# Optimization experiments

Hardware: AMD Instinct MI355X
Metric: run time of the kernel (lower is better)

The kernel has to match this reference:

```python
import jax, jax.numpy as jnp
import numpy as np

N_NODES = 50000
D = 128
N_POS = 400000
N_NEG = 200000  # N_NODES * neg_k(4)
E = N_POS + N_NEG


def setup_inputs() -> dict:
    key = jax.random.key(0)
    k_x, k_w1, k_w2, k_p = jax.random.split(key, 4)
    x = jax.random.normal(k_x, (N_NODES, D), dtype=jnp.float32)
    # torch nn.Linear params: y = x @ W.T + b
    W1 = jax.random.normal(k_w1, (D, 2 * D), dtype=jnp.float32) * (1.0 / np.sqrt(2 * D))
    b1 = jnp.zeros((D,), dtype=jnp.float32)
    W2 = jax.random.normal(k_w2, (1, D), dtype=jnp.float32) * (1.0 / np.sqrt(D))
    b2 = jnp.zeros((1,), dtype=jnp.float32)
    pairs = jax.random.randint(k_p, (2, E), 0, N_NODES, dtype=jnp.int64)
    labels = jnp.concatenate([jnp.ones((N_POS,), jnp.float32), jnp.zeros((N_NEG,), jnp.float32)])
    return {"x": x, "W1": W1, "b1": b1, "W2": W2, "b2": b2, "labels": labels, "pairs": pairs}


def reference(x, W1, b1, W2, b2, labels, pairs):
    us, vs = pairs[0], pairs[1]
    # edge gather + concat: [E, 2D]
    feats = jnp.concatenate([x[us], x[vs]], axis=-1)
    h = jax.nn.relu(feats @ W1.T + b1)            # [E, D]
    z = (h @ W2.T + b2).ravel()                   # [E] logits
    # binary_cross_entropy_with_logits, mean reduction (numerically stable)
    loss = -jnp.mean(labels * jax.nn.log_sigmoid(z) + (1.0 - labels) * jax.nn.log_sigmoid(-z))
    return loss
```

## Files before the change

kernel.cpp:

```cpp
#include <hip/hip_runtime.h>
#include <hip/hip_fp16.h>

#define D 128
#define TWO_D 256

typedef _Float16 half2v __attribute__((ext_vector_type(2)));
typedef _Float16 half8v __attribute__((ext_vector_type(8)));
typedef float floatx4 __attribute__((ext_vector_type(4)));
typedef unsigned int uintx4 __attribute__((ext_vector_type(4)));

__device__ inline unsigned int pkrtz(float a, float b) {
    return __builtin_bit_cast(unsigned int, __builtin_amdgcn_cvt_pkrtz(a, b));
}

__global__ void build_wtf(const float* __restrict__ W1,
                          unsigned short* __restrict__ Wtf) {
    const int id = blockIdx.x * 256 + threadIdx.x;
    const int lane = id & 63, ks = (id >> 6) & 3, t = (id >> 8) & 3, w = id >> 10;
    const int quad = lane >> 4, l16 = lane & 15;
    const int o = w * 64 + t * 16 + l16;
    const float* wrow = (o < D) ? (W1 + (size_t)o * TWO_D)
                                : (W1 + (size_t)(o - D) * TWO_D + D);
    const float* wp = wrow + ks * 32 + quad * 8;
    floatx4 w0 = *(const floatx4*)wp;
    floatx4 w1v = *(const floatx4*)(wp + 4);
    uint4 pk;
    pk.x = pkrtz(w0[0], w0[1]);  pk.y = pkrtz(w0[2], w0[3]);
    pk.z = pkrtz(w1v[0], w1v[1]); pk.w = pkrtz(w1v[2], w1v[3]);
    *(uint4*)(Wtf + (size_t)id * 8) = pk;
}

__global__ __launch_bounds__(256) void gemm_nodes(
        const float* __restrict__ x, const unsigned short* __restrict__ Wtf,
        const float* __restrict__ b1,
        unsigned char* __restrict__ AB, float* __restrict__ out0, int nNodes) {
    const int tid  = threadIdx.x;
    const int wave = tid >> 6, lane = tid & 63;
    const int quad = lane >> 4, l16 = lane & 15;
    const int nb0  = blockIdx.x * 64;

    if (blockIdx.x == 0 && tid == 0) *out0 = 0.f;

    half8v Bf[4][4];
    float bias[4];
#pragma unroll
    for (int t = 0; t < 4; ++t) {
        const int o = wave * 64 + t * 16 + l16;
        bias[t] = (o < D) ? b1[o] : 0.f;
#pragma unroll
        for (int ks = 0; ks < 4; ++ks)
            Bf[t][ks] = *(const half8v*)(Wtf +
                ((size_t)(((wave * 4 + t) * 4 + ks) * 64) + lane) * 8);
    }

    __shared__ __align__(16) unsigned short xs[64][136];
    __shared__ __align__(16) float ct[2][16][260];

#pragma unroll
    for (int i = 0; i < 4; ++i) {
        const int c = tid + 256 * i;
        const int row = c >> 4, col8 = c & 15;
        const int node = nb0 + row;
        const int nc = node < nNodes ? node : nNodes - 1;
        const float* xp = x + (size_t)nc * D + col8 * 8;
        floatx4 v0 = *(const floatx4*)xp;
        floatx4 v1 = *(const floatx4*)(xp + 4);
        uint4 pk;
        pk.x = pkrtz(v0[0], v0[1]);  pk.y = pkrtz(v0[2], v0[3]);
        pk.z = pkrtz(v1[0], v1[1]);  pk.w = pkrtz(v1[2], v1[3]);
        *(uint4*)&xs[row][col8 * 8] = pk;
    }
    __syncthreads();

    const int srow = tid >> 4;
    const int sc8  = tid & 15;

    for (int sub = 0; sub < 4; ++sub) {
        half8v Af[4];
#pragma unroll
        for (int ks = 0; ks < 4; ++ks)
            Af[ks] = *(const half8v*)&xs[sub * 16 + l16][ks * 32 + quad * 8];

        floatx4 acc[4];
#pragma unroll
        for (int t = 0; t < 4; ++t) acc[t] = (floatx4){0.f, 0.f, 0.f, 0.f};
#pragma unroll
        for (int ks = 0; ks < 4; ++ks)
#pragma unroll
            for (int t = 0; t < 4; ++t)
                acc[t] = __builtin_amdgcn_mfma_f32_16x16x32_f16(Af[ks], Bf[t][ks], acc[t], 0, 0, 0);

        float (*cts)[260] = ct[sub & 1];
#pragma unroll
        for (int t = 0; t < 4; ++t) {
            const int o = wave * 64 + t * 16 + l16;
#pragma unroll
            for (int r = 0; r < 4; ++r)
                cts[quad * 4 + r][o] = acc[t][r] + bias[t];
        }
        __syncthreads();

        const int nrow = nb0 + sub * 16 + srow;
        if (nrow < nNodes) {
            floatx4 f0 = *(const floatx4*)&cts[srow][sc8 * 16];
            floatx4 f1 = *(const floatx4*)&cts[srow][sc8 * 16 + 4];
            floatx4 f2 = *(const floatx4*)&cts[srow][sc8 * 16 + 8];
            floatx4 f3 = *(const floatx4*)&cts[srow][sc8 * 16 + 12];
            uint4 o8;
            int d;
            d = __builtin_amdgcn_cvt_pk_fp8_f32(f0[0], f0[1], 0, false);
            d = __builtin_amdgcn_cvt_pk_fp8_f32(f0[2], f0[3], d, true);
            o8.x = (unsigned int)d;
            d = __builtin_amdgcn_cvt_pk_fp8_f32(f1[0], f1[1], 0, false);
            d = __builtin_amdgcn_cvt_pk_fp8_f32(f1[2], f1[3], d, true);
            o8.y = (unsigned int)d;
            d = __builtin_amdgcn_cvt_pk_fp8_f32(f2[0], f2[1], 0, false);
            d = __builtin_amdgcn_cvt_pk_fp8_f32(f2[2], f2[3], d, true);
            o8.z = (unsigned int)d;
            d = __builtin_amdgcn_cvt_pk_fp8_f32(f3[0], f3[1], 0, false);
            d = __builtin_amdgcn_cvt_pk_fp8_f32(f3[2], f3[3], d, true);
            o8.w = (unsigned int)d;
            *(uint4*)(AB + (size_t)nrow * TWO_D + sc8 * 16) = o8;
        }
    }
}

__device__ inline float dot4_fp8(unsigned int wa, unsigned int wb,
                                 unsigned int w2lo, unsigned int w2hi, float z) {
#if __has_builtin(__builtin_amdgcn_cvt_pk_f16_fp8)
    half2v a01 = __builtin_bit_cast(half2v, __builtin_amdgcn_cvt_pk_f16_fp8((short)(wa & 0xffffu)));
    half2v a23 = __builtin_bit_cast(half2v, __builtin_amdgcn_cvt_pk_f16_fp8((short)(wa >> 16)));
    half2v b01 = __builtin_bit_cast(half2v, __builtin_amdgcn_cvt_pk_f16_fp8((short)(wb & 0xffffu)));
    half2v b23 = __builtin_bit_cast(half2v, __builtin_amdgcn_cvt_pk_f16_fp8((short)(wb >> 16)));
    half2v zero = {(_Float16)0, (_Float16)0};
    half2v s01 = __builtin_elementwise_max(a01 + b01, zero);
    half2v s23 = __builtin_elementwise_max(a23 + b23, zero);
    z = __builtin_amdgcn_fdot2(s01, __builtin_bit_cast(half2v, w2lo), z, false);
    z = __builtin_amdgcn_fdot2(s23, __builtin_bit_cast(half2v, w2hi), z, false);
#else
    auto a01 = __builtin_amdgcn_cvt_pk_f32_fp8(wa, false);
    auto a23 = __builtin_amdgcn_cvt_pk_f32_fp8(wa, true);
    auto b01 = __builtin_amdgcn_cvt_pk_f32_fp8(wb, false);
    auto b23 = __builtin_amdgcn_cvt_pk_f32_fp8(wb, true);
    half2v wlo = __builtin_bit_cast(half2v, w2lo);
    half2v whi = __builtin_bit_cast(half2v, w2hi);
    float s0 = fmaxf(a01[0] + b01[0], 0.f), s1 = fmaxf(a01[1] + b01[1], 0.f);
    float s2 = fmaxf(a23[0] + b23[0], 0.f), s3 = fmaxf(a23[1] + b23[1], 0.f);
    z = fmaf(s0, (float)wlo[0], z); z = fmaf(s1, (float)wlo[1], z);
    z = fmaf(s2, (float)whi[0], z); z = fmaf(s3, (float)whi[1], z);
#endif
    return z;
}

__device__ inline float dot16(const uintx4 a4, const uintx4 b4,
                              const uintx4 w2a, const uintx4 w2b) {
    float z = 0.f;
    z = dot4_fp8(a4[0], b4[0], w2a[0], w2a[1], z);
    z = dot4_fp8(a4[1], b4[1], w2a[2], w2a[3], z);
    z = dot4_fp8(a4[2], b4[2], w2b[0], w2b[1], z);
    z = dot4_fp8(a4[3], b4[3], w2b[2], w2b[3], z);
    return z;
}

__device__ inline float red8(float z) {
    z += __shfl_xor(z, 4, 8);
    z += __shfl_xor(z, 2, 8);
    z += __shfl_xor(z, 1, 8);
    return z;
}

__device__ inline float bce(float z, float y) {
    const float t = __expf(-fabsf(z));
    return fmaxf(z, 0.f) - z * y + __logf(1.f + t);
}

__global__ __launch_bounds__(256) void edge_loss(
        const unsigned char* __restrict__ AB,
        const int* __restrict__ pairs,
        const float* __restrict__ labels,
        const float* __restrict__ W2,
        const float* __restrict__ b2,
        float* __restrict__ out, int E, float invE) {
    __shared__ unsigned int w2p[64];
    const int tid = threadIdx.x;
    if (tid < 64) {
        float2 w = *(const float2*)(W2 + tid * 2);
        half2v p = { (_Float16)w.x, (_Float16)w.y };
        w2p[tid] = __builtin_bit_cast(unsigned int, p);
    }
    __syncthreads();
    const int l8   = tid & 7;
    const uintx4 w2a = *(const uintx4*)&w2p[l8 * 8];
    const uintx4 w2b = *(const uintx4*)&w2p[l8 * 8 + 4];
    const float bb2 = b2[0];

    float acc = 0.f;
    const int group = (blockIdx.x * 256 + tid) >> 3;
    const int e0 = group * 8;
    if (e0 < E) {
        const int4 ua = *(const int4*)(pairs + e0);
        const int4 ub = *(const int4*)(pairs + e0 + 4);
        const int4 va = *(const int4*)(pairs + E + e0);
        const int4 vb = *(const int4*)(pairs + E + e0 + 4);
        const float lab = labels[e0 + l8];
        const int us[8] = {ua.x, ua.y, ua.z, ua.w, ub.x, ub.y, ub.z, ub.w};
        const int vs[8] = {va.x, va.y, va.z, va.w, vb.x, vb.y, vb.z, vb.w};

        unsigned int offA[8], offB[8];
#pragma unroll
        for (int k = 0; k < 8; ++k) {
            offA[k] = (unsigned int)us[k] * TWO_D + l8 * 16;
            offB[k] = (unsigned int)vs[k] * TWO_D + D + l8 * 16;
        }

        uintx4 A[8], B[8];
#pragma unroll
        for (int k = 0; k < 8; ++k) {
            asm volatile("global_load_dwordx4 %0, %1, %2"
                         : "=v"(A[k]) : "v"(offA[k]), "s"(AB) : "memory");
            asm volatile("global_load_dwordx4 %0, %1, %2"
                         : "=v"(B[k]) : "v"(offB[k]), "s"(AB) : "memory");
        }

        float z[8];
#define CONS2(k0, k1, cnt)                                                   \
        asm volatile("s_waitcnt vmcnt(" cnt ")" ::: "memory");               \
        __builtin_amdgcn_sched_barrier(0);                                   \
        z[k0] = red8(dot16(A[k0], B[k0], w2a, w2b));                         \
        z[k1] = red8(dot16(A[k1], B[k1], w2a, w2b));
        CONS2(0, 1, "12")
        CONS2(2, 3, "8")
        CONS2(4, 5, "4")
        CONS2(6, 7, "0")
#undef CONS2

        float zsel = z[0];
#pragma unroll
        for (int k = 1; k < 8; ++k)
            if (l8 == k) zsel = z[k];
        acc = bce(zsel + bb2, lab);
    }

#pragma unroll
    for (int m = 32; m >= 1; m >>= 1) acc += __shfl_xor(acc, m, 64);
    __shared__ float red[4];
    if ((tid & 63) == 0) red[tid >> 6] = acc;
    __syncthreads();
    if (tid == 0)
        atomicAdd(out, (red[0] + red[1] + red[2] + red[3]) * invE);
}

extern "C" void kernel_launch(void* const* d_in, const int* in_sizes, int n_in,
                              void* d_out, int out_size, void* d_ws, size_t ws_size,
                              hipStream_t stream) {
    const float* x      = (const float*)d_in[0];
    const float* W1     = (const float*)d_in[1];
    const float* b1     = (const float*)d_in[2];
    const float* W2     = (const float*)d_in[3];
    const float* b2     = (const float*)d_in[4];
    const float* labels = (const float*)d_in[5];
    const int*   pairs  = (const int*)d_in[6];

    const int nNodes = in_sizes[0] / D;
    const int E      = in_sizes[5];

    unsigned char*  AB  = (unsigned char*)d_ws;
    unsigned short* Wtf = (unsigned short*)((char*)d_ws + 13000704);

    build_wtf<<<16, 256, 0, stream>>>(W1, Wtf);
    gemm_nodes<<<(nNodes + 63) / 64, 256, 0, stream>>>(x, Wtf, b1, AB,
                                                        (float*)d_out, nNodes);
    const int nGroups = (E + 7) / 8;
    const int nBlocks = (nGroups + 31) / 32;
    edge_loss<<<nBlocks, 256, 0, stream>>>(AB, pairs, labels, W2, b2,
                                           (float*)d_out, E, 1.0f / (float)E);
}
```

Before: 125.1 us.

## Bucket edges by source-node bin so source features are staged in LDS

Result: slower. 170.7 us (+36.4%).

```diff
diff --git a/kernel.cpp b/kernel.cpp
--- a/kernel.cpp
+++ b/kernel.cpp
@@ -3,6 +3,14 @@
 
 #define D 128
 #define TWO_D 256
+#define BINW 128
+
+#define AB_OFF      0
+#define WTF_OFF     13000704
+#define HIST_OFF    13066240
+#define PSTART_OFF  13068288
+#define PCUR_OFF    13070336
+#define REC_OFF     13120512
 
 typedef _Float16 half2v __attribute__((ext_vector_type(2)));
 typedef _Float16 half8v __attribute__((ext_vector_type(8)));
@@ -14,8 +22,10 @@
 }
 
 __global__ void build_wtf(const float* __restrict__ W1,
-                          unsigned short* __restrict__ Wtf) {
+                          unsigned short* __restrict__ Wtf,
+                          int* __restrict__ hist, int nbins) {
     const int id = blockIdx.x * 256 + threadIdx.x;
+    if (id < nbins) hist[id] = 0;
     const int lane = id & 63, ks = (id >> 6) & 3, t = (id >> 8) & 3, w = id >> 10;
     const int quad = lane >> 4, l16 = lane & 15;
     const int o = w * 64 + t * 16 + l16;
@@ -124,6 +134,56 @@
         }
     }
 }
+
+
+__global__ __launch_bounds__(256) void hist_k(
+        const int* __restrict__ pairs, int* __restrict__ hist,
+        int E, int nbins) {
+    __shared__ int lh[512];
+    const int tid = threadIdx.x;
+    for (int i = tid; i < nbins; i += 256) lh[i] = 0;
+    __syncthreads();
+    const int stride = gridDim.x * 256;
+    for (int e = blockIdx.x * 256 + tid; e < E; e += stride)
+        atomicAdd(&lh[pairs[e] >> 7], 1);
+    __syncthreads();
+    for (int i = tid; i < nbins; i += 256)
+        if (lh[i]) atomicAdd(&hist[i], lh[i]);
+}
+
+__global__ __launch_bounds__(512) void scan_k(
+        const int* __restrict__ hist, int* __restrict__ pstart,
+        int* __restrict__ pcur, int nbins) {
+    __shared__ int sv[512];
+    const int t = threadIdx.x;
+    const int v = (t < nbins) ? ((hist[t] + 7) & ~7) : 0;
+    sv[t] = v;
+    for (int s = 1; s < 512; s <<= 1) {
+        __syncthreads();
+        const int a = (t >= s) ? sv[t - s] : 0;
+        __syncthreads();
+        sv[t] += a;
+    }
+    __syncthreads();
+    const int excl = sv[t] - v;
+    if (t < nbins) { pstart[t] = excl; pcur[t * 32] = excl; }
+}
+
+__global__ __launch_bounds__(256) void scatter_k(
+        const int* __restrict__ pairs, const float* __restrict__ labels,
+        int* __restrict__ pcur, unsigned int* __restrict__ rec,
+        int E) {
+    const int stride = gridDim.x * 256;
+    for (int e = blockIdx.x * 256 + threadIdx.x; e < E; e += stride) {
+        const int u = pairs[e];
+        const unsigned int v = (unsigned int)pairs[E + e];
+        const unsigned int lb = (labels[e] > 0.5f) ? 0x80000000u : 0u;
+        const int b = u >> 7;
+        const int slot = atomicAdd(&pcur[b * 32], 1);
+        rec[slot] = v | ((unsigned int)(u & 127) << 16) | lb;
+    }
+}
+
 
 __device__ inline float dot4_fp8(unsigned int wa, unsigned int wb,
                                  unsigned int w2lo, unsigned int w2hi, float z) {
@@ -176,69 +236,95 @@
 
 __global__ __launch_bounds__(256) void edge_loss(
         const unsigned char* __restrict__ AB,
-        const int* __restrict__ pairs,
-        const float* __restrict__ labels,
+        const unsigned int* __restrict__ rec,
+        const int* __restrict__ hist,
+        const int* __restrict__ pstart,
         const float* __restrict__ W2,
         const float* __restrict__ b2,
-        float* __restrict__ out, int E, float invE) {
+        float* __restrict__ out, int nNodes, float invE) {
+    const int tid = threadIdx.x;
+    const int b   = blockIdx.x >> 1;
+    const int h   = blockIdx.x & 1;
+
+    __shared__ __align__(16) unsigned char xs[BINW * 128];
     __shared__ unsigned int w2p[64];
-    const int tid = threadIdx.x;
+
     if (tid < 64) {
         float2 w = *(const float2*)(W2 + tid * 2);
         half2v p = { (_Float16)w.x, (_Float16)w.y };
         w2p[tid] = __builtin_bit_cast(unsigned int, p);
     }
-    __syncthreads();
-    const int l8   = tid & 7;
+    {
+        const int row = tid >> 1, half = tid & 1;
+        const size_t src = (size_t)(b * BINW + row) * TWO_D + half * 64;
+#pragma unroll
+        for (int j = 0; j < 4; ++j)
+            *(uint4*)&xs[tid * 64 + j * 16] =
+                *(const uint4*)(AB + src + j * 16);
+    }
+    __syncthreads();
+
+    const int l8 = tid & 7, tg = tid >> 3;
     const uintx4 w2a = *(const uintx4*)&w2p[l8 * 8];
     const uintx4 w2b = *(const uintx4*)&w2p[l8 * 8 + 4];
     const float bb2 = b2[0];
 
+    const int cnt = hist[b];
+    const int ps  = pstart[b];
+    const int ng  = (cnt + 7) >> 3;
+    const int nj  = (ng + 1 - h) >> 1;
+    const int nit = (nj + 31) >> 5;
+
     float acc = 0.f;
-    const int group = (blockIdx.x * 256 + tid) >> 3;
-    const int e0 = group * 8;
-    if (e0 < E) {
-        const int4 ua = *(const int4*)(pairs + e0);
-        const int4 ub = *(const int4*)(pairs + e0 + 4);
-        const int4 va = *(const int4*)(pairs + E + e0);
-        const int4 vb = *(const int4*)(pairs + E + e0 + 4);
-        const float lab = labels[e0 + l8];
-        const int us[8] = {ua.x, ua.y, ua.z, ua.w, ub.x, ub.y, ub.z, ub.w};
-        const int vs[8] = {va.x, va.y, va.z, va.w, vb.x, vb.y, vb.z, vb.w};
-
-        unsigned int offA[8], offB[8];
-#pragma unroll
-        for (int k = 0; k < 8; ++k) {
-            offA[k] = (unsigned int)us[k] * TWO_D + l8 * 16;
-            offB[k] = (unsigned int)vs[k] * TWO_D + D + l8 * 16;
-        }
-
-        uintx4 A[8], B[8];
-#pragma unroll
-        for (int k = 0; k < 8; ++k) {
-            asm volatile("global_load_dwordx4 %0, %1, %2"
-                         : "=v"(A[k]) : "v"(offA[k]), "s"(AB) : "memory");
+    for (int it = 0; it < nit; ++it) {
+        const int j  = it * 32 + tg;
+        const int jc = (j < nj) ? j : (nj - 1);
+        const int g  = 2 * jc + h;
+        const int slot0 = ps + g * 8;
+
+        const uint4 r0 = *(const uint4*)(rec + slot0);
+        const uint4 r1 = *(const uint4*)(rec + slot0 + 4);
+        const unsigned int rc[8] = {r0.x, r0.y, r0.z, r0.w,
+                                    r1.x, r1.y, r1.z, r1.w};
+
+        unsigned int offB[8];
+#pragma unroll
+        for (int k = 0; k < 8; ++k)
+            offB[k] = (rc[k] & 0xffffu) * TWO_D + D + l8 * 16;
+
+        uintx4 B[8];
+#pragma unroll
+        for (int k = 0; k < 8; ++k)
             asm volatile("global_load_dwordx4 %0, %1, %2"
                          : "=v"(B[k]) : "v"(offB[k]), "s"(AB) : "memory");
+
+        uintx4 A[8];
+#pragma unroll
+        for (int k = 0; k < 8; ++k) {
+            const int row = (rc[k] >> 16) & 127;
+            A[k] = *(const uintx4*)&xs[row * 128 + l8 * 16];
         }
 
         float z[8];
-#define CONS2(k0, k1, cnt)                                                   \
-        asm volatile("s_waitcnt vmcnt(" cnt ")" ::: "memory");               \
+#define CONS2(k0, k1, cnt_s)                                                 \
+        asm volatile("s_waitcnt vmcnt(" cnt_s ")" ::: "memory");             \
         __builtin_amdgcn_sched_barrier(0);                                   \
         z[k0] = red8(dot16(A[k0], B[k0], w2a, w2b));                         \
         z[k1] = red8(dot16(A[k1], B[k1], w2a, w2b));
-        CONS2(0, 1, "12")
-        CONS2(2, 3, "8")
-        CONS2(4, 5, "4")
+        CONS2(0, 1, "6")
+        CONS2(2, 3, "4")
+        CONS2(4, 5, "2")
         CONS2(6, 7, "0")
 #undef CONS2
 
         float zsel = z[0];
+        unsigned int rsel = rc[0];
 #pragma unroll
         for (int k = 1; k < 8; ++k)
-            if (l8 == k) zsel = z[k];
-        acc = bce(zsel + bb2, lab);
+            if (l8 == k) { zsel = z[k]; rsel = rc[k]; }
+        const float lab = (rsel & 0x80000000u) ? 1.f : 0.f;
+        const bool valid = (j < nj) && (g * 8 + l8 < cnt);
+        acc += valid ? bce(zsel + bb2, lab) : 0.f;
     }
 
 #pragma unroll
@@ -263,15 +349,23 @@
 
     const int nNodes = in_sizes[0] / D;
     const int E      = in_sizes[5];
-
-    unsigned char*  AB  = (unsigned char*)d_ws;
-    unsigned short* Wtf = (unsigned short*)((char*)d_ws + 13000704);
-
-    build_wtf<<<16, 256, 0, stream>>>(W1, Wtf);
+    const int nbins  = (nNodes + BINW - 1) / BINW;
+
+    char* ws = (char*)d_ws;
+    unsigned char*  AB     = (unsigned char*)(ws + AB_OFF);
+    unsigned short* Wtf    = (unsigned short*)(ws + WTF_OFF);
+    int*            hist   = (int*)(ws + HIST_OFF);
+    int*            pstart = (int*)(ws + PSTART_OFF);
+    int*            pcur   = (int*)(ws + PCUR_OFF);
+    unsigned int*   recp   = (unsigned int*)(ws + REC_OFF);
+
+    build_wtf<<<16, 256, 0, stream>>>(W1, Wtf, hist, nbins);
     gemm_nodes<<<(nNodes + 63) / 64, 256, 0, stream>>>(x, Wtf, b1, AB,
                                                         (float*)d_out, nNodes);
-    const int nGroups = (E + 7) / 8;
-    const int nBlocks = (nGroups + 31) / 32;
-    edge_loss<<<nBlocks, 256, 0, stream>>>(AB, pairs, labels, W2, b2,
-                                           (float*)d_out, E, 1.0f / (float)E);
-}
+    hist_k<<<256, 256, 0, stream>>>(pairs, hist, E, nbins);
+    scan_k<<<1, 512, 0, stream>>>(hist, pstart, pcur, nbins);
+    scatter_k<<<512, 256, 0, stream>>>(pairs, labels, pcur, recp, E);
+    edge_loss<<<nbins * 2, 256, 0, stream>>>(AB, recp, hist, pstart, W2, b2,
+                                             (float*)d_out, nNodes,
+                                             1.0f / (float)E);
+}
```

## Write fp8 node projections directly from MFMA registers with permuted column layout

Applied to the files above, without the earlier changes.

Result: no change. 126.3 us (+1.0%).

```diff
diff --git a/kernel.cpp b/kernel.cpp
--- a/kernel.cpp
+++ b/kernel.cpp
@@ -54,7 +54,6 @@
     }
 
     __shared__ __align__(16) unsigned short xs[64][136];
-    __shared__ __align__(16) float ct[2][16][260];
 
 #pragma unroll
     for (int i = 0; i < 4; ++i) {
@@ -72,9 +71,6 @@
     }
     __syncthreads();
 
-    const int srow = tid >> 4;
-    const int sc8  = tid & 15;
-
     for (int sub = 0; sub < 4; ++sub) {
         half8v Af[4];
 #pragma unroll
@@ -90,37 +86,18 @@
             for (int t = 0; t < 4; ++t)
                 acc[t] = __builtin_amdgcn_mfma_f32_16x16x32_f16(Af[ks], Bf[t][ks], acc[t], 0, 0, 0);
 
-        float (*cts)[260] = ct[sub & 1];
-#pragma unroll
-        for (int t = 0; t < 4; ++t) {
-            const int o = wave * 64 + t * 16 + l16;
-#pragma unroll
-            for (int r = 0; r < 4; ++r)
-                cts[quad * 4 + r][o] = acc[t][r] + bias[t];
-        }
-        __syncthreads();
-
-        const int nrow = nb0 + sub * 16 + srow;
-        if (nrow < nNodes) {
-            floatx4 f0 = *(const floatx4*)&cts[srow][sc8 * 16];
-            floatx4 f1 = *(const floatx4*)&cts[srow][sc8 * 16 + 4];
-            floatx4 f2 = *(const floatx4*)&cts[srow][sc8 * 16 + 8];
-            floatx4 f3 = *(const floatx4*)&cts[srow][sc8 * 16 + 12];
-            uint4 o8;
-            int d;
-            d = __builtin_amdgcn_cvt_pk_fp8_f32(f0[0], f0[1], 0, false);
-            d = __builtin_amdgcn_cvt_pk_fp8_f32(f0[2], f0[3], d, true);
-            o8.x = (unsigned int)d;
-            d = __builtin_amdgcn_cvt_pk_fp8_f32(f1[0], f1[1], 0, false);
-            d = __builtin_amdgcn_cvt_pk_fp8_f32(f1[2], f1[3], d, true);
-            o8.y = (unsigned int)d;
-            d = __builtin_amdgcn_cvt_pk_fp8_f32(f2[0], f2[1], 0, false);
-            d = __builtin_amdgcn_cvt_pk_fp8_f32(f2[2], f2[3], d, true);
-            o8.z = (unsigned int)d;
-            d = __builtin_amdgcn_cvt_pk_fp8_f32(f3[0], f3[1], 0, false);
-            d = __builtin_amdgcn_cvt_pk_fp8_f32(f3[2], f3[3], d, true);
-            o8.w = (unsigned int)d;
-            *(uint4*)(AB + (size_t)nrow * TWO_D + sc8 * 16) = o8;
+#pragma unroll
+        for (int r = 0; r < 4; ++r) {
+            const int nrow = nb0 + sub * 16 + quad * 4 + r;
+            if (nrow < nNodes) {
+                int d;
+                d = __builtin_amdgcn_cvt_pk_fp8_f32(acc[0][r] + bias[0],
+                                                    acc[1][r] + bias[1], 0, false);
+                d = __builtin_amdgcn_cvt_pk_fp8_f32(acc[2][r] + bias[2],
+                                                    acc[3][r] + bias[3], d, true);
+                *(unsigned int*)(AB + (size_t)nrow * TWO_D + wave * 64 + l16 * 4) =
+                    (unsigned int)d;
+            }
         }
     }
 }
@@ -184,8 +161,10 @@
     __shared__ unsigned int w2p[64];
     const int tid = threadIdx.x;
     if (tid < 64) {
-        float2 w = *(const float2*)(W2 + tid * 2);
-        half2v p = { (_Float16)w.x, (_Float16)w.y };
+        const int b0 = 2 * tid, b1 = 2 * tid + 1;
+        const int j0 = (b0 >> 6) * 64 + (b0 & 3) * 16 + ((b0 & 63) >> 2);
+        const int j1 = (b1 >> 6) * 64 + (b1 & 3) * 16 + ((b1 & 63) >> 2);
+        half2v p = { (_Float16)W2[j0], (_Float16)W2[j1] };
         w2p[tid] = __builtin_bit_cast(unsigned int, p);
     }
     __syncthreads();
```
